# Optimization experiments

Measured on AMD Instinct MI355X. Metric: run time of the kernel, lower is better.

The kernel has to match this reference:

```python
import jax, jax.numpy as jnp
import numpy as np

N_NODES = 100000
N_EDGES = 1600000
IN_DIM = 128
OUT_DIM = 128
ORDER = 2
EPS = 1e-9


def setup_inputs() -> dict:
    key = jax.random.key(0)
    ks = jax.random.split(key, 4)
    features = jax.random.normal(ks[0], (N_NODES, IN_DIM), dtype=jnp.float32)
    src = jax.random.randint(ks[1], (N_EDGES,), 0, N_NODES)
    dst = jax.random.randint(ks[2], (N_EDGES,), 0, N_NODES)
    w = jnp.ones((N_EDGES,), dtype=jnp.float32)
    D_norm = jax.random.uniform(ks[3], (N_NODES, 1), dtype=jnp.float32)
    # xavier-normal-ish init for the order+1 linear weights
    Wk = jax.random.split(jax.random.key(1), ORDER + 1)
    std = np.sqrt(2.0 / (IN_DIM + OUT_DIM)).astype(np.float32)
    W = jnp.stack([jax.random.normal(k, (OUT_DIM, IN_DIM), dtype=jnp.float32) * std for k in Wk])
    b = jnp.zeros((ORDER + 1, OUT_DIM), dtype=jnp.float32)
    scale = jnp.ones((ORDER + 1, OUT_DIM), dtype=jnp.float32)
    offset = jnp.zeros((ORDER + 1, OUT_DIM), dtype=jnp.float32)
    return {"features": features, "src": src, "dst": dst, "w": w,
            "D_norm": D_norm, "W": W, "b": b, "scale": scale, "offset": offset}


def reference(features, src, dst, w, D_norm, W, b, scale, offset):
    N = features.shape[0]

    def feat_trans(ft, i):
        h = ft @ W[i].T + b[i]          # [N, out]
        h = jax.nn.relu(h)
        mean = jnp.mean(h, axis=1, keepdims=True)
        var = jnp.var(h, axis=1, keepdims=True) + EPS  # unbiased=False
        return (h - mean) * scale[i] * jax.lax.rsqrt(var) + offset[i]

    h_hop = [features]
    for _ in range(ORDER):
        m = h_hop[-1][src] * w[:, None]                 # u_mul_e gather  [E, d]
        agg = jax.ops.segment_sum(m, dst, num_segments=N)  # sum reduce to dst
        h_hop.append(agg * D_norm)

    h_part = [feat_trans(ft, i) for i, ft in enumerate(h_hop)]
    return jnp.concatenate(h_part, axis=1)  # aggr='concat' -> [N, (order+1)*out]
```

## Files before the change

### kernel.cpp

```cpp
#include <hip/hip_runtime.h>
#include <hip/hip_bf16.h>

#define OUT_STRIDE 384
#define EPSV 1e-9f
#define BSH 9
#define BS 512
#define NBMAX 512
#define CH 4096

typedef __attribute__((ext_vector_type(8))) short bf16x8;
typedef __attribute__((ext_vector_type(4))) float f32x4;

static __device__ __forceinline__ unsigned short f2bf(float f) {
    __hip_bfloat16 h = __float2bfloat16(f);
    return *reinterpret_cast<unsigned short*>(&h);
}

__global__ __launch_bounds__(256)
void multisplit_pack_kernel(const int* __restrict__ src, const int* __restrict__ dst,
                            const float* __restrict__ w, int* __restrict__ bcur,
                            int2* __restrict__ edw, unsigned short* __restrict__ dlu,
                            int E, int CAP,
                            const float* __restrict__ features,
                            unsigned short* __restrict__ featb, long n4) {
    __shared__ int hist[NBMAX], scan_[NBMAX], gbase[NBMAX], lcur[NBMAX];
    __shared__ int recS[CH * 3];
    __shared__ int wt[4];
    const int t = threadIdx.x;
    const int lane = t & 63, wv = t >> 6;
    const int c0 = blockIdx.x * CH;
    const int cnt_total = min(CH, E - c0);

    for (int i = t; i < NBMAX; i += 256) hist[i] = 0;
    __syncthreads();
    #pragma unroll
    for (int p = 0; p < CH / 256; ++p) {
        int i = c0 + p * 256 + t;
        if (i < E) atomicAdd(&hist[dst[i] >> BSH], 1);
    }
    __syncthreads();
    {
        int b0 = 2 * t, b1 = 2 * t + 1;
        int h0 = hist[b0], h1 = hist[b1];
        int s = h0 + h1;
        int inc = s;
        #pragma unroll
        for (int d = 1; d < 64; d <<= 1) { int u = __shfl_up(inc, d); if (lane >= d) inc += u; }
        if (lane == 63) wt[wv] = inc;
        __syncthreads();
        int base = 0;
        for (int w2 = 0; w2 < wv; ++w2) base += wt[w2];
        int ex = base + inc - s;
        scan_[b0] = ex;
        scan_[b1] = ex + h0;
    }
    __syncthreads();
    for (int i = t; i < NBMAX; i += 256) {
        if (hist[i] > 0) gbase[i] = atomicAdd(&bcur[i], hist[i]);
        lcur[i] = scan_[i];
    }
    __syncthreads();
    #pragma unroll
    for (int p = 0; p < CH / 256; ++p) {
        int i = c0 + p * 256 + t;
        if (i < E) {
            int d = dst[i];
            int b = d >> BSH;
            int j = atomicAdd(&lcur[b], 1);
            recS[3 * j]     = src[i];
            recS[3 * j + 1] = d;
            recS[3 * j + 2] = __float_as_int(w[i]);
        }
    }
    __syncthreads();
    #pragma unroll
    for (int p = 0; p < CH / 256; ++p) {
        int j = p * 256 + t;
        if (j < cnt_total) {
            int d = recS[3 * j + 1];
            int b = d >> BSH;
            int g = gbase[b] + (j - scan_[b]);
            if (g < CAP) {
                long gp = (long)b * CAP + g;
                edw[gp] = make_int2(recS[3 * j], recS[3 * j + 2]);
                dlu[gp] = (unsigned short)(d - (b << BSH));
            }
        }
    }
    long gid = blockIdx.x * blockDim.x + threadIdx.x;
    long stride = (long)gridDim.x * blockDim.x;
    for (long p = gid; p < n4; p += stride) {
        float4 v = ((const float4*)features)[p];
        ushort4 o;
        o.x = f2bf(v.x); o.y = f2bf(v.y); o.z = f2bf(v.z); o.w = f2bf(v.w);
        *(ushort4*)&featb[p * 4] = o;
    }
}

__global__ __launch_bounds__(256)
void bucket_csr_kernel(const int2* __restrict__ edw, const unsigned short* __restrict__ dlu,
                       const int* __restrict__ bcur,
                       int* __restrict__ off, int* __restrict__ deg,
                       int2* __restrict__ ed, int N, int CAP) {
    __shared__ int h[BS];
    __shared__ int wt[4];
    const int b = blockIdx.x;
    const int t = threadIdx.x;
    const int lane = t & 63, wv = t >> 6;
    const int cnt = min(bcur[b], CAP);
    const long base = (long)b * CAP;
    const int n0 = b << BSH;
    const int nn = min(BS, N - n0);

    for (int i = t; i < BS; i += 256) h[i] = 0;
    __syncthreads();
    for (int i = t; i < cnt; i += 256) atomicAdd(&h[dlu[base + i]], 1);
    __syncthreads();
    {
        int j0 = 2 * t;
        int l0 = h[j0], l1 = h[j0 + 1];
        int s = l0 + l1;
        int inc = s;
        #pragma unroll
        for (int d = 1; d < 64; d <<= 1) { int u = __shfl_up(inc, d); if (lane >= d) inc += u; }
        if (lane == 63) wt[wv] = inc;
        __syncthreads();
        int base_ = 0;
        for (int w2 = 0; w2 < wv; ++w2) base_ += wt[w2];
        int ex = base_ + inc - s;
        int e0 = ex, e1 = ex + l0;
        __syncthreads();
        h[j0] = e0; h[j0 + 1] = e1;
        if (j0 < nn)     { off[n0 + j0]     = (int)(base + e0); deg[n0 + j0]     = l0; }
        if (j0 + 1 < nn) { off[n0 + j0 + 1] = (int)(base + e1); deg[n0 + j0 + 1] = l1; }
    }
    __syncthreads();
    for (int i = t; i < cnt; i += 256) {
        int d = dlu[base + i];
        int pos = atomicAdd(&h[d], 1);
        ed[base + pos] = edw[base + i];
    }
}

__device__ __forceinline__ void acc8(float* a, int4 r, float w) {
    #pragma unroll
    for (int j = 0; j < 4; ++j) {
        int bits = (&r.x)[j];
        float f0 = __int_as_float(bits << 16);
        float f1 = __int_as_float(bits & 0xffff0000);
        a[2 * j]     += f0 * w;
        a[2 * j + 1] += f1 * w;
    }
}

__device__ __forceinline__ int2 nt_ld_int2(const int2* p) {
    long v = __builtin_nontemporal_load((const long*)p);
    int2 r; r.x = (int)(v & 0xffffffffL); r.y = (int)(((unsigned long)v) >> 32);
    return r;
}

__global__ __launch_bounds__(256)
void gather_wave(const unsigned short* __restrict__ X,
                 const int* __restrict__ off, const int* __restrict__ deg,
                 const int2* __restrict__ ed,
                 const float* __restrict__ Dn,
                 unsigned short* __restrict__ outb, int N) {
    const int tid = threadIdx.x;
    const int n = blockIdx.x * 4 + (tid >> 6);
    if (n >= N) return;
    const int lane = tid & 63;
    const int g2 = lane >> 4;
    const int l = lane & 15;
    const int beg = __builtin_nontemporal_load(&off[n]);
    const int end = beg + __builtin_nontemporal_load(&deg[n]);
    float a[8] = {0.f, 0.f, 0.f, 0.f, 0.f, 0.f, 0.f, 0.f};
    const unsigned short* Xc = X + 8 * l;
    int i = beg + g2;
    for (; i + 12 < end; i += 16) {
        int2 e0 = nt_ld_int2(&ed[i]);
        int2 e1 = nt_ld_int2(&ed[i + 4]);
        int2 e2 = nt_ld_int2(&ed[i + 8]);
        int2 e3 = nt_ld_int2(&ed[i + 12]);
        int4 r0 = *(const int4*)(Xc + (long)e0.x * 128);
        int4 r1 = *(const int4*)(Xc + (long)e1.x * 128);
        int4 r2 = *(const int4*)(Xc + (long)e2.x * 128);
        int4 r3 = *(const int4*)(Xc + (long)e3.x * 128);
        acc8(a, r0, __int_as_float(e0.y));
        acc8(a, r1, __int_as_float(e1.y));
        acc8(a, r2, __int_as_float(e2.y));
        acc8(a, r3, __int_as_float(e3.y));
    }
    for (; i < end; i += 4) {
        int2 e0 = nt_ld_int2(&ed[i]);
        int4 r0 = *(const int4*)(Xc + (long)e0.x * 128);
        acc8(a, r0, __int_as_float(e0.y));
    }
    #pragma unroll
    for (int j = 0; j < 8; ++j) {
        a[j] += __shfl_xor(a[j], 16);
        a[j] += __shfl_xor(a[j], 32);
    }
    if (g2 == 0) {
        const float dn = Dn[n];
        int4 o;
        #pragma unroll
        for (int j = 0; j < 4; ++j) {
            unsigned lo = f2bf(a[2 * j] * dn);
            unsigned hi = f2bf(a[2 * j + 1] * dn);
            (&o.x)[j] = (int)((hi << 16) | lo);
        }
        *(int4*)&outb[(long)n * 128 + 8 * l] = o;
    }
}

#define XS 136

__device__ __forceinline__ void stage_W(const float* __restrict__ Wf_hop, short* Wl, int tid) {
    const float4* W4 = (const float4*)Wf_hop;
    for (int idx = tid; idx < 128 * 32; idx += 256) {
        float4 v = W4[idx];
        int row = idx >> 5;
        int col = (idx & 31) * 4;
        short* p = &Wl[row * XS + col];
        p[0] = f2bf(v.x); p[1] = f2bf(v.y); p[2] = f2bf(v.z); p[3] = f2bf(v.w);
    }
}

__device__ __forceinline__ void mfma_ln_epilogue(
    const short* Xl, const short* Wl,
    const float* __restrict__ bp, const float* __restrict__ sp, const float* __restrict__ op,
    float* out, int ocol, int n0, int N, int tid)
{
    const int lane = tid & 63;
    const int wv = tid >> 6;
    f32x4 acc[8];
    #pragma unroll
    for (int c = 0; c < 8; ++c) acc[c] = (f32x4){0.f, 0.f, 0.f, 0.f};
    const int rsub = lane & 15;
    const int g = lane >> 4;
    const short* xbase = &Xl[(wv * 16 + rsub) * XS + g * 8];
    const short* wbase = &Wl[rsub * XS + g * 8];
    #pragma unroll
    for (int kk = 0; kk < 4; ++kk) {
        bf16x8 a = *(const bf16x8*)(xbase + kk * 32);
        #pragma unroll
        for (int c = 0; c < 8; ++c) {
            bf16x8 bb = *(const bf16x8*)(wbase + c * 16 * XS + kk * 32);
            acc[c] = __builtin_amdgcn_mfma_f32_16x16x32_bf16(a, bb, acc[c], 0, 0, 0);
        }
    }
    float sum[4] = {0.f, 0.f, 0.f, 0.f};
    float ssq[4] = {0.f, 0.f, 0.f, 0.f};
    #pragma unroll
    for (int c = 0; c < 8; ++c) {
        float bias = bp[c * 16 + rsub];
        #pragma unroll
        for (int r = 0; r < 4; ++r) {
            float h = acc[c][r] + bias;
            h = fmaxf(h, 0.0f);
            acc[c][r] = h;
            sum[r] += h;
            ssq[r] += h * h;
        }
    }
    #pragma unroll
    for (int msk = 1; msk < 16; msk <<= 1) {
        #pragma unroll
        for (int r = 0; r < 4; ++r) {
            sum[r] += __shfl_xor(sum[r], msk);
            ssq[r] += __shfl_xor(ssq[r], msk);
        }
    }
    #pragma unroll
    for (int r = 0; r < 4; ++r) {
        int n = n0 + wv * 16 + g * 4 + r;
        if (n >= N) continue;
        float mean = sum[r] * (1.0f / 128.0f);
        float var = ssq[r] * (1.0f / 128.0f) - mean * mean + EPSV;
        float inv = rsqrtf(var);
        float* orow = out + (long)n * OUT_STRIDE + ocol;
        #pragma unroll
        for (int c = 0; c < 8; ++c) {
            int col = c * 16 + rsub;
            __builtin_nontemporal_store((acc[c][r] - mean) * sp[col] * inv + op[col], &orow[col]);
        }
    }
}

__global__ __launch_bounds__(256)
void transform3_kernel(const unsigned short* __restrict__ featb,
                       const unsigned short* __restrict__ h1b,
                       const unsigned short* __restrict__ h2b,
                       const float* __restrict__ Wf,
                       const float* __restrict__ bf, const float* __restrict__ scf,
                       const float* __restrict__ offp,
                       float* out, int N)
{
    const int hop = blockIdx.y;
    const int tid = threadIdx.x;
    __shared__ __attribute__((aligned(16))) short Wl[128 * XS];
    __shared__ __attribute__((aligned(16))) short Xl[64 * XS];
    stage_W(Wf + (long)hop * 128 * 128, Wl, tid);
    const unsigned short* xb = (hop == 0) ? featb : (hop == 1) ? h1b : h2b;
    #pragma unroll
    for (int t2 = 0; t2 < 2; ++t2) {
        const int n0 = (blockIdx.x * 2 + t2) * 64;
        for (int idx = tid; idx < 64 * 16; idx += 256) {
            int r = idx >> 4;
            int c = (idx & 15) * 8;
            int n = n0 + r;
            int4 v = make_int4(0, 0, 0, 0);
            if (n < N) v = *(const int4*)(xb + (long)n * 128 + c);
            *(int4*)&Xl[r * XS + c] = v;
        }
        __syncthreads();
        mfma_ln_epilogue(Xl, Wl, bf + hop * 128, scf + hop * 128, offp + hop * 128,
                         out, hop * 128, n0, N, tid);
        __syncthreads();
    }
}

__global__ __launch_bounds__(256)
void scatter_kernel(const float* X, long xstride, long xcol0,
                    const int* __restrict__ src, const int* __restrict__ dst,
                    const float* __restrict__ w, const float* __restrict__ Dn,
                    int useDn, float* out, long ocol0, int nE)
{
    const int lane = threadIdx.x & 63;
    const int wave = (int)((blockIdx.x * blockDim.x + threadIdx.x) >> 6);
    const int nWaves = (int)((gridDim.x * blockDim.x) >> 6);
    for (int e = wave; e < nE; e += nWaves) {
        const int s = src[e];
        const int d = dst[e];
        float ww = w[e];
        if (useDn) ww *= Dn[s];
        const float2 v = *(const float2*)(X + (long)s * xstride + xcol0 + 2 * lane);
        float* o = out + (long)d * OUT_STRIDE + ocol0 + 2 * lane;
        atomicAdd(o, v.x * ww);
        atomicAdd(o + 1, v.y * ww);
    }
}

__global__ __launch_bounds__(256)
void transform_f32_kernel(const float* x, long xs, int useDnIn,
                          const float* __restrict__ Dn,
                          const float* __restrict__ Wf_hop,
                          const float* __restrict__ bp, const float* __restrict__ sp,
                          const float* __restrict__ op,
                          float* out, int ocol, int N)
{
    __shared__ __attribute__((aligned(16))) short Wl[128 * XS];
    __shared__ __attribute__((aligned(16))) short Xl[64 * XS];
    const int tid = threadIdx.x;
    stage_W(Wf_hop, Wl, tid);
    const int n0 = blockIdx.x * 64;
    for (int idx = tid; idx < 64 * 32; idx += 256) {
        int r = idx >> 5;
        int col = (idx & 31) * 4;
        int n = n0 + r;
        float4 v = make_float4(0.f, 0.f, 0.f, 0.f);
        float m = 1.0f;
        if (n < N) {
            v = *(const float4*)(x + (long)n * xs + col);
            if (useDnIn) m = Dn[n];
        }
        short* p = &Xl[r * XS + col];
        p[0] = f2bf(v.x * m); p[1] = f2bf(v.y * m); p[2] = f2bf(v.z * m); p[3] = f2bf(v.w * m);
    }
    __syncthreads();
    mfma_ln_epilogue(Xl, Wl, bp, sp, op, out, ocol, n0, N, tid);
}

extern "C" void kernel_launch(void* const* d_in, const int* in_sizes, int n_in,
                              void* d_out, int out_size, void* d_ws, size_t ws_size,
                              hipStream_t stream) {
    const float* features = (const float*)d_in[0];
    const int*   src      = (const int*)d_in[1];
    const int*   dst      = (const int*)d_in[2];
    const float* w        = (const float*)d_in[3];
    const float* Dn       = (const float*)d_in[4];
    const float* W        = (const float*)d_in[5];
    const float* b        = (const float*)d_in[6];
    const float* scale    = (const float*)d_in[7];
    const float* offset   = (const float*)d_in[8];
    float* out = (float*)d_out;
    const int N = in_sizes[0] / 128;
    const int E = in_sizes[1];
    const int NB = (N + BS - 1) >> BSH;
    const int nblk = (N + 63) / 64;
    int CAP = ((E / (NB > 0 ? NB : 1)) * 3 / 2 + 255) & ~255;
    if (CAP < 1024) CAP = 1024;
    const size_t NC = (size_t)NB * CAP;

    const size_t o_off = 0;
    const size_t o_deg = (size_t)N;
    const size_t o_ed  = ((size_t)2 * N + 3) & ~(size_t)3;
    const size_t o_bc  = o_ed + 2 * NC;
    const size_t o_un  = (o_bc + NB + 3) & ~(size_t)3;
    const size_t o_dl  = o_un + 2 * NC;
    const size_t o_fb  = (o_dl + (NC + 1) / 2 + 3) & ~(size_t)3;
    const size_t need  = (o_fb + 3 * (size_t)64 * N) * 4;

    if (NB <= NBMAX && ws_size >= need) {
        int* ws_i  = (int*)d_ws;
        int* off   = ws_i + o_off;
        int* deg   = ws_i + o_deg;
        int2* ed   = (int2*)(ws_i + o_ed);
        int* bcur  = ws_i + o_bc;
        int2* edw  = (int2*)(ws_i + o_un);
        unsigned short* dlu = (unsigned short*)(ws_i + o_dl);
        unsigned short* featb = (unsigned short*)(ws_i + o_fb);
        unsigned short* h1b   = featb + (size_t)N * 128;
        unsigned short* h2b   = h1b + (size_t)N * 128;

        hipMemsetAsync(bcur, 0, (size_t)NB * 4, stream);
        multisplit_pack_kernel<<<(E + CH - 1) / CH, 256, 0, stream>>>(
            src, dst, w, bcur, edw, dlu, E, CAP, features, featb, (long)N * 32);
        bucket_csr_kernel<<<NB, 256, 0, stream>>>(edw, dlu, bcur, off, deg, ed, N, CAP);

        gather_wave<<<(N + 3) / 4, 256, 0, stream>>>(featb, off, deg, ed, Dn, h1b, N);
        gather_wave<<<(N + 3) / 4, 256, 0, stream>>>(h1b, off, deg, ed, Dn, h2b, N);

        dim3 tg((N + 127) / 128, 3);
        transform3_kernel<<<tg, 256, 0, stream>>>(featb, h1b, h2b, W, b, scale, offset, out, N);
    } else {
        hipMemsetAsync(out, 0, (size_t)out_size * sizeof(float), stream);
        scatter_kernel<<<2048, 256, 0, stream>>>(features, 128, 0, src, dst, w, Dn, 0, out, 128, E);
        scatter_kernel<<<2048, 256, 0, stream>>>(out, OUT_STRIDE, 128, src, dst, w, Dn, 1, out, 256, E);
        transform_f32_kernel<<<nblk, 256, 0, stream>>>(features, 128, 0, Dn, W, b, scale, offset, out, 0, N);
        transform_f32_kernel<<<nblk, 256, 0, stream>>>(out + 128, OUT_STRIDE, 1, Dn, W + 128 * 128, b + 128, scale + 128, offset + 128, out, 128, N);
        transform_f32_kernel<<<nblk, 256, 0, stream>>>(out + 256, OUT_STRIDE, 1, Dn, W + 2 * 128 * 128, b + 256, scale + 256, offset + 256, out, 256, N);
    }
}
```

Baseline: 306.6 us.

## Fuse neighbor gather with MFMA transform and LayerNorm epilogue per hop

Replaces the two standalone gather kernels and the three-hop transform kernel with one fused kernel per hop. Each 512-thread block gathers 64 destination rows into shared memory, with waves taking rows dynamically through a shared atomic counter. It then runs the bf16 MFMA GEMM and the normalization epilogue, splitting output columns across two wave halves. This removes the h2 buffer round trip and separate transform launches. In exchange, the W staging and gather now sit in the same block, which may cut occupancy and overlap.

```diff
diff --git a/kernel.cpp b/kernel.cpp
--- a/kernel.cpp
+++ b/kernel.cpp
@@ -7,6 +7,7 @@
 #define BS 512
 #define NBMAX 512
 #define CH 4096
+#define XS 136
 
 typedef __attribute__((ext_vector_type(8))) short bf16x8;
 typedef __attribute__((ext_vector_type(4))) float f32x4;
@@ -159,61 +160,176 @@
     return r;
 }
 
-__global__ __launch_bounds__(256)
-void gather_wave(const unsigned short* __restrict__ X,
-                 const int* __restrict__ off, const int* __restrict__ deg,
-                 const int2* __restrict__ ed,
-                 const float* __restrict__ Dn,
-                 unsigned short* __restrict__ outb, int N) {
+__device__ __forceinline__ void stage_W_512(const float* __restrict__ Wf_hop, short* Wl, int tid) {
+    const float4* W4 = (const float4*)Wf_hop;
+    for (int idx = tid; idx < 128 * 32; idx += 512) {
+        float4 v = W4[idx];
+        int row = idx >> 5;
+        int col = (idx & 31) * 4;
+        short* p = &Wl[row * XS + col];
+        p[0] = f2bf(v.x); p[1] = f2bf(v.y); p[2] = f2bf(v.z); p[3] = f2bf(v.w);
+    }
+}
+
+__global__ __launch_bounds__(512)
+void fusedT_kernel(const unsigned short* __restrict__ xsrc,
+                   const int* __restrict__ off, const int* __restrict__ deg,
+                   const int2* __restrict__ ed,
+                   const float* __restrict__ Dn,
+                   const float* __restrict__ Wf_hop,
+                   const float* __restrict__ bp, const float* __restrict__ sp,
+                   const float* __restrict__ op,
+                   unsigned short* __restrict__ rowout,
+                   float* __restrict__ out, int ocol, int N, int DO_GATHER)
+{
+    __shared__ __attribute__((aligned(16))) short Wl[128 * XS];
+    __shared__ __attribute__((aligned(16))) short Xl[64 * XS];
+    __shared__ float sums[64][2], ssqs[64][2];
+    __shared__ int cur;
     const int tid = threadIdx.x;
-    const int n = blockIdx.x * 4 + (tid >> 6);
-    if (n >= N) return;
     const int lane = tid & 63;
-    const int g2 = lane >> 4;
-    const int l = lane & 15;
-    const int beg = __builtin_nontemporal_load(&off[n]);
-    const int end = beg + __builtin_nontemporal_load(&deg[n]);
-    float a[8] = {0.f, 0.f, 0.f, 0.f, 0.f, 0.f, 0.f, 0.f};
-    const unsigned short* Xc = X + 8 * l;
-    int i = beg + g2;
-    for (; i + 12 < end; i += 16) {
-        int2 e0 = nt_ld_int2(&ed[i]);
-        int2 e1 = nt_ld_int2(&ed[i + 4]);
-        int2 e2 = nt_ld_int2(&ed[i + 8]);
-        int2 e3 = nt_ld_int2(&ed[i + 12]);
-        int4 r0 = *(const int4*)(Xc + (long)e0.x * 128);
-        int4 r1 = *(const int4*)(Xc + (long)e1.x * 128);
-        int4 r2 = *(const int4*)(Xc + (long)e2.x * 128);
-        int4 r3 = *(const int4*)(Xc + (long)e3.x * 128);
-        acc8(a, r0, __int_as_float(e0.y));
-        acc8(a, r1, __int_as_float(e1.y));
-        acc8(a, r2, __int_as_float(e2.y));
-        acc8(a, r3, __int_as_float(e3.y));
-    }
-    for (; i < end; i += 4) {
-        int2 e0 = nt_ld_int2(&ed[i]);
-        int4 r0 = *(const int4*)(Xc + (long)e0.x * 128);
-        acc8(a, r0, __int_as_float(e0.y));
-    }
-    #pragma unroll
-    for (int j = 0; j < 8; ++j) {
-        a[j] += __shfl_xor(a[j], 16);
-        a[j] += __shfl_xor(a[j], 32);
-    }
-    if (g2 == 0) {
-        const float dn = Dn[n];
-        int4 o;
-        #pragma unroll
-        for (int j = 0; j < 4; ++j) {
-            unsigned lo = f2bf(a[2 * j] * dn);
-            unsigned hi = f2bf(a[2 * j + 1] * dn);
-            (&o.x)[j] = (int)((hi << 16) | lo);
-        }
-        *(int4*)&outb[(long)n * 128 + 8 * l] = o;
-    }
-}
-
-#define XS 136
+    const int n0 = blockIdx.x * 64;
+
+    if (tid == 0) cur = 0;
+    stage_W_512(Wf_hop, Wl, tid);
+    __syncthreads();
+
+    if (DO_GATHER) {
+        const int g2 = lane >> 4;
+        const int l = lane & 15;
+        const unsigned short* Xc = xsrc + 8 * l;
+        for (;;) {
+            int q;
+            if (lane == 0) q = atomicAdd(&cur, 1);
+            q = __shfl(q, 0);
+            if (q >= 64) break;
+            const int n = n0 + q;
+            if (n >= N) {
+                if (g2 == 0) *(int4*)&Xl[q * XS + 8 * l] = make_int4(0, 0, 0, 0);
+                continue;
+            }
+            const int beg = __builtin_nontemporal_load(&off[n]);
+            const int end = beg + __builtin_nontemporal_load(&deg[n]);
+            float a[8] = {0.f, 0.f, 0.f, 0.f, 0.f, 0.f, 0.f, 0.f};
+            int i = beg + g2;
+            for (; i + 12 < end; i += 16) {
+                int2 e0 = nt_ld_int2(&ed[i]);
+                int2 e1 = nt_ld_int2(&ed[i + 4]);
+                int2 e2 = nt_ld_int2(&ed[i + 8]);
+                int2 e3 = nt_ld_int2(&ed[i + 12]);
+                int4 r0 = *(const int4*)(Xc + (long)e0.x * 128);
+                int4 r1 = *(const int4*)(Xc + (long)e1.x * 128);
+                int4 r2 = *(const int4*)(Xc + (long)e2.x * 128);
+                int4 r3 = *(const int4*)(Xc + (long)e3.x * 128);
+                acc8(a, r0, __int_as_float(e0.y));
+                acc8(a, r1, __int_as_float(e1.y));
+                acc8(a, r2, __int_as_float(e2.y));
+                acc8(a, r3, __int_as_float(e3.y));
+            }
+            for (; i < end; i += 4) {
+                int2 e0 = nt_ld_int2(&ed[i]);
+                int4 r0 = *(const int4*)(Xc + (long)e0.x * 128);
+                acc8(a, r0, __int_as_float(e0.y));
+            }
+            #pragma unroll
+            for (int j = 0; j < 8; ++j) {
+                a[j] += __shfl_xor(a[j], 16);
+                a[j] += __shfl_xor(a[j], 32);
+            }
+            if (g2 == 0) {
+                const float dn = Dn[n];
+                int4 o;
+                #pragma unroll
+                for (int j = 0; j < 4; ++j) {
+                    unsigned lo = f2bf(a[2 * j] * dn);
+                    unsigned hi = f2bf(a[2 * j + 1] * dn);
+                    (&o.x)[j] = (int)((hi << 16) | lo);
+                }
+                *(int4*)&Xl[q * XS + 8 * l] = o;
+                if (rowout) *(int4*)&rowout[(long)n * 128 + 8 * l] = o;
+            }
+        }
+    } else {
+        for (int idx = tid; idx < 64 * 16; idx += 512) {
+            int r = idx >> 4;
+            int c = (idx & 15) * 8;
+            int n = n0 + r;
+            int4 v = make_int4(0, 0, 0, 0);
+            if (n < N) v = *(const int4*)(xsrc + (long)n * 128 + c);
+            *(int4*)&Xl[r * XS + c] = v;
+        }
+    }
+    __syncthreads();
+
+    const int wv = tid >> 6;
+    const int wv2 = wv & 3;
+    const int half = wv >> 2;
+    const int ch = half * 64;
+    const int rsub = lane & 15;
+    const int g = lane >> 4;
+    f32x4 acc[4];
+    #pragma unroll
+    for (int c = 0; c < 4; ++c) acc[c] = (f32x4){0.f, 0.f, 0.f, 0.f};
+    const short* xbase = &Xl[(wv2 * 16 + rsub) * XS + g * 8];
+    const short* wbase = &Wl[(ch + rsub) * XS + g * 8];
+    #pragma unroll
+    for (int kk = 0; kk < 4; ++kk) {
+        bf16x8 a = *(const bf16x8*)(xbase + kk * 32);
+        #pragma unroll
+        for (int c = 0; c < 4; ++c) {
+            bf16x8 bb = *(const bf16x8*)(wbase + c * 16 * XS + kk * 32);
+            acc[c] = __builtin_amdgcn_mfma_f32_16x16x32_bf16(a, bb, acc[c], 0, 0, 0);
+        }
+    }
+    float sum[4] = {0.f, 0.f, 0.f, 0.f};
+    float ssq[4] = {0.f, 0.f, 0.f, 0.f};
+    #pragma unroll
+    for (int c = 0; c < 4; ++c) {
+        float bias = bp[ch + c * 16 + rsub];
+        #pragma unroll
+        for (int r = 0; r < 4; ++r) {
+            float h = acc[c][r] + bias;
+            h = fmaxf(h, 0.0f);
+            acc[c][r] = h;
+            sum[r] += h;
+            ssq[r] += h * h;
+        }
+    }
+    #pragma unroll
+    for (int msk = 1; msk < 16; msk <<= 1) {
+        #pragma unroll
+        for (int r = 0; r < 4; ++r) {
+            sum[r] += __shfl_xor(sum[r], msk);
+            ssq[r] += __shfl_xor(ssq[r], msk);
+        }
+    }
+    if (rsub == 0) {
+        #pragma unroll
+        for (int r = 0; r < 4; ++r) {
+            int row = wv2 * 16 + g * 4 + r;
+            sums[row][half] = sum[r];
+            ssqs[row][half] = ssq[r];
+        }
+    }
+    __syncthreads();
+    #pragma unroll
+    for (int r = 0; r < 4; ++r) {
+        int row = wv2 * 16 + g * 4 + r;
+        int n = n0 + row;
+        if (n >= N) continue;
+        float S = sums[row][0] + sums[row][1];
+        float Q = ssqs[row][0] + ssqs[row][1];
+        float mean = S * (1.0f / 128.0f);
+        float var = Q * (1.0f / 128.0f) - mean * mean + EPSV;
+        float inv = rsqrtf(var);
+        float* orow = out + (long)n * OUT_STRIDE + ocol;
+        #pragma unroll
+        for (int c = 0; c < 4; ++c) {
+            int col = ch + c * 16 + rsub;
+            __builtin_nontemporal_store((acc[c][r] - mean) * sp[col] * inv + op[col], &orow[col]);
+        }
+    }
+}
 
 __device__ __forceinline__ void stage_W(const float* __restrict__ Wf_hop, short* Wl, int tid) {
     const float4* W4 = (const float4*)Wf_hop;
@@ -282,41 +398,8 @@
         #pragma unroll
         for (int c = 0; c < 8; ++c) {
             int col = c * 16 + rsub;
-            __builtin_nontemporal_store((acc[c][r] - mean) * sp[col] * inv + op[col], &orow[col]);
-        }
-    }
-}
-
-__global__ __launch_bounds__(256)
-void transform3_kernel(const unsigned short* __restrict__ featb,
-                       const unsigned short* __restrict__ h1b,
-                       const unsigned short* __restrict__ h2b,
-                       const float* __restrict__ Wf,
-                       const float* __restrict__ bf, const float* __restrict__ scf,
-                       const float* __restrict__ offp,
-                       float* out, int N)
-{
-    const int hop = blockIdx.y;
-    const int tid = threadIdx.x;
-    __shared__ __attribute__((aligned(16))) short Wl[128 * XS];
-    __shared__ __attribute__((aligned(16))) short Xl[64 * XS];
-    stage_W(Wf + (long)hop * 128 * 128, Wl, tid);
-    const unsigned short* xb = (hop == 0) ? featb : (hop == 1) ? h1b : h2b;
-    #pragma unroll
-    for (int t2 = 0; t2 < 2; ++t2) {
-        const int n0 = (blockIdx.x * 2 + t2) * 64;
-        for (int idx = tid; idx < 64 * 16; idx += 256) {
-            int r = idx >> 4;
-            int c = (idx & 15) * 8;
-            int n = n0 + r;
-            int4 v = make_int4(0, 0, 0, 0);
-            if (n < N) v = *(const int4*)(xb + (long)n * 128 + c);
-            *(int4*)&Xl[r * XS + c] = v;
-        }
-        __syncthreads();
-        mfma_ln_epilogue(Xl, Wl, bf + hop * 128, scf + hop * 128, offp + hop * 128,
-                         out, hop * 128, n0, N, tid);
-        __syncthreads();
+            orow[col] = (acc[c][r] - mean) * sp[col] * inv + op[col];
+        }
     }
 }
 
@@ -399,7 +482,7 @@
     const size_t o_un  = (o_bc + NB + 3) & ~(size_t)3;
     const size_t o_dl  = o_un + 2 * NC;
     const size_t o_fb  = (o_dl + (NC + 1) / 2 + 3) & ~(size_t)3;
-    const size_t need  = (o_fb + 3 * (size_t)64 * N) * 4;
+    const size_t need  = (o_fb + 2 * (size_t)64 * N) * 4;
 
     if (NB <= NBMAX && ws_size >= need) {
         int* ws_i  = (int*)d_ws;
@@ -411,18 +494,18 @@
         unsigned short* dlu = (unsigned short*)(ws_i + o_dl);
         unsigned short* featb = (unsigned short*)(ws_i + o_fb);
         unsigned short* h1b   = featb + (size_t)N * 128;
-        unsigned short* h2b   = h1b + (size_t)N * 128;
 
         hipMemsetAsync(bcur, 0, (size_t)NB * 4, stream);
         multisplit_pack_kernel<<<(E + CH - 1) / CH, 256, 0, stream>>>(
             src, dst, w, bcur, edw, dlu, E, CAP, features, featb, (long)N * 32);
         bucket_csr_kernel<<<NB, 256, 0, stream>>>(edw, dlu, bcur, off, deg, ed, N, CAP);
 
-        gather_wave<<<(N + 3) / 4, 256, 0, stream>>>(featb, off, deg, ed, Dn, h1b, N);
-        gather_wave<<<(N + 3) / 4, 256, 0, stream>>>(h1b, off, deg, ed, Dn, h2b, N);
-
-        dim3 tg((N + 127) / 128, 3);
-        transform3_kernel<<<tg, 256, 0, stream>>>(featb, h1b, h2b, W, b, scale, offset, out, N);
+        fusedT_kernel<<<nblk, 512, 0, stream>>>(featb, off, deg, ed, Dn,
+            W + 128 * 128, b + 128, scale + 128, offset + 128, h1b, out, 128, N, 1);
+        fusedT_kernel<<<nblk, 512, 0, stream>>>(h1b, off, deg, ed, Dn,
+            W + 2 * 128 * 128, b + 256, scale + 256, offset + 256, nullptr, out, 256, N, 1);
+        fusedT_kernel<<<nblk, 512, 0, stream>>>(featb, off, deg, ed, Dn,
+            W, b, scale, offset, nullptr, out, 0, N, 0);
     } else {
         hipMemsetAsync(out, 0, (size_t)out_size * sizeof(float), stream);
         scatter_kernel<<<2048, 256, 0, stream>>>(features, 128, 0, src, dst, w, Dn, 0, out, 128, E);
```

Measured after the change: 352.3 us. 1.15x slower.
